# Performance work log

Measured on AMD Instinct MI355X. Metric: run time of the kernel, lower is better.

## Reference

```python
import jax, jax.numpy as jnp
import numpy as np

B, T, F, C, H = 128, 2048, 16, 8, 20  # batch, seq_len, n_features, n_channels, mlp_hidden


def _iir(u, b, rho, psi):
    """Stable 2nd-order MIMO IIR (dynoNet parametrization).
    u: [B,T,I], b: [O,I,3], rho/psi: [O,I,1] -> returns [B,T,O].
    y[t] = v[t] - a1*y[t-1] - a2*y[t-2] per (o,i) pair, summed over i.
    """
    r = jax.nn.sigmoid(rho[..., 0])            # [O,I]
    beta = jnp.pi * jax.nn.sigmoid(psi[..., 0])
    a1 = -2.0 * r * jnp.cos(beta)              # [O,I]
    a2 = r * r                                 # [O,I]
    up = jnp.pad(u, ((0, 0), (2, 0), (0, 0)))  # causal pad, up[:,2:]==u
    # FIR numerator v[b,t,o,i] = sum_k b[o,i,k] * u[b,t-k,i]
    v = (b[:, :, 0] * u[:, :, None, :]
         + b[:, :, 1] * up[:, 1:-1, None, :]
         + b[:, :, 2] * up[:, :-2, None, :])   # [B,T,O,I]

    def step(carry, vt):
        y1, y2 = carry
        y = vt - a1 * y1 - a2 * y2
        return (y, y1), y

    Bn, O, I = u.shape[0], b.shape[0], b.shape[1]
    z = jnp.zeros((Bn, O, I), u.dtype)
    _, ys = jax.lax.scan(step, (z, z), jnp.moveaxis(v, 1, 0))  # [T,B,O,I]
    return jnp.moveaxis(ys.sum(-1), 0, 1)      # [B,T,O]


def setup_inputs() -> dict:
    key = jax.random.key(0)
    ks = jax.random.split(key, 9)
    return {
        "x": jax.random.normal(ks[0], (B, T, F), jnp.float32),
        # G1: n_features -> n_channels
        "b1": 0.01 * jax.random.normal(ks[1], (C, F, 3), jnp.float32),
        "rho1": 0.1 * jax.random.normal(ks[2], (C, F, 1), jnp.float32),
        "psi1": 0.1 * jax.random.normal(ks[3], (C, F, 1), jnp.float32),
        # MLP: Linear(C,H) -> Tanh -> Linear(H,C)
        "w1": jax.random.normal(ks[4], (H, C), jnp.float32) / np.sqrt(C),
        "bias1": jnp.zeros((H,), jnp.float32),
        "w2": jax.random.normal(ks[5], (C, H), jnp.float32) / np.sqrt(H),
        "bias2": jnp.zeros((C,), jnp.float32),
        # G2: n_channels -> 1
        "b2": 0.01 * jax.random.normal(ks[6], (1, C, 3), jnp.float32),
        "rho2": 0.1 * jax.random.normal(ks[7], (1, C, 1), jnp.float32),
        "psi2": 0.1 * jax.random.normal(ks[8], (1, C, 1), jnp.float32),
    }


def reference(x, b1, rho1, psi1, w1, bias1, w2, bias2, b2, rho2, psi2):
    y1 = _iir(x, b1, rho1, psi1)                 # [B,T,C]
    h = jnp.tanh(y1 @ w1.T + bias1)              # [B,T,H]
    y2 = h @ w2.T + bias2                        # [B,T,C]
    y3 = _iir(y2, b2, rho2, psi2)                # [B,T,1]
    return y3[:, -1, :]                          # [B,1]
```

## Files before the change

kernel.cpp:

```cpp
#include <hip/hip_runtime.h>
#include <math.h>

#define BATCH 128
#define TLEN  2048
#define FDIM  16
#define CDIM  8
#define HDIM  20
#define KTAPS 64
#define XWIN  128
#define XSTR  132

__device__ float g_filt[8192 + 512];

__global__ void wh_precompute(const float* __restrict__ b1,
                              const float* __restrict__ rho1,
                              const float* __restrict__ psi1,
                              const float* __restrict__ b2,
                              const float* __restrict__ rho2,
                              const float* __restrict__ psi2) {
    int tid = threadIdx.x;
    if (tid >= 136) return;
    float c0, c1, c2, rho, psi;
    if (tid < 128) {
        int oi = tid;
        c0 = b1[oi * 3 + 0]; c1 = b1[oi * 3 + 1]; c2 = b1[oi * 3 + 2];
        rho = rho1[oi]; psi = psi1[oi];
    } else {
        int c = tid - 128;
        c0 = b2[c * 3 + 0]; c1 = b2[c * 3 + 1]; c2 = b2[c * 3 + 2];
        rho = rho2[c]; psi = psi2[c];
    }
    float r    = 1.0f / (1.0f + expf(-rho));
    float beta = 3.14159265358979323846f * (1.0f / (1.0f + expf(-psi)));
    float a1   = -2.0f * r * cosf(beta);
    float a2   = r * r;

    float ym1 = 0.0f, ym2 = 0.0f;
    for (int t = 0; t < KTAPS; ++t) {
        float v = (t == 0) ? c0 : (t == 1) ? c1 : (t == 2) ? c2 : 0.0f;
        float y = v - a1 * ym1 - a2 * ym2;
        if (tid < 128) {
            int o = tid >> 4, i = tid & 15;
            g_filt[(i * KTAPS + (KTAPS - 1 - t)) * CDIM + o] = y;
        } else {
            int c = tid - 128;
            g_filt[8192 + c * KTAPS + t] = y;
        }
        ym2 = ym1; ym1 = y;
    }
}

__global__ __launch_bounds__(256) void wh_main(const float* __restrict__ x,
                                               const float* __restrict__ w1,
                                               const float* __restrict__ bias1,
                                               const float* __restrict__ w2,
                                               const float* __restrict__ bias2,
                                               float* __restrict__ out) {
    __shared__ float xs[FDIM * XSTR];
    __shared__ float part[4 * CDIM * 64];

    const int tid  = threadIdx.x;
    const int b    = blockIdx.x;
    const int lane = tid & 63;
    const int w    = tid >> 6;

    const float* xb = x + ((size_t)b * TLEN + (TLEN - XWIN)) * FDIM;
#pragma unroll
    for (int rep = 0; rep < 2; ++rep) {
        int f4 = tid + rep * 256;
        float4 v = ((const float4*)xb)[f4];
        int lt = f4 >> 2;
        int ib = (f4 & 3) * 4;
        xs[(ib + 0) * XSTR + lt] = v.x;
        xs[(ib + 1) * XSTR + lt] = v.y;
        xs[(ib + 2) * XSTR + lt] = v.z;
        xs[(ib + 3) * XSTR + lt] = v.w;
    }
    __syncthreads();

    float acc[CDIM];
#pragma unroll
    for (int o = 0; o < CDIM; ++o) acc[o] = 0.0f;

#pragma unroll
    for (int ii = 0; ii < 4; ++ii) {
        int i = (w << 2) + ii;
        const float* xrow = &xs[i * XSTR + lane + 1];
        const float* kp = g_filt + __builtin_amdgcn_readfirstlane(i * (KTAPS * CDIM));
#pragma unroll 8
        for (int s = 0; s < KTAPS; ++s) {
            float xv = xrow[s];
#pragma unroll
            for (int o = 0; o < CDIM; ++o) acc[o] += kp[s * CDIM + o] * xv;
        }
    }

#pragma unroll
    for (int o = 0; o < CDIM; ++o) part[(w * CDIM + o) * 64 + lane] = acc[o];
    __syncthreads();

    if (w == 0) {
        float y1v[CDIM];
#pragma unroll
        for (int o = 0; o < CDIM; ++o)
            y1v[o] = part[(0 * CDIM + o) * 64 + lane] + part[(1 * CDIM + o) * 64 + lane] +
                     part[(2 * CDIM + o) * 64 + lane] + part[(3 * CDIM + o) * 64 + lane];

        float y2v[CDIM];
#pragma unroll
        for (int c = 0; c < CDIM; ++c) y2v[c] = bias2[c];
#pragma unroll
        for (int j = 0; j < HDIM; ++j) {
            float a = bias1[j];
#pragma unroll
            for (int o = 0; o < CDIM; ++o) a += w1[j * CDIM + o] * y1v[o];
            float hv = tanhf(a);
#pragma unroll
            for (int c = 0; c < CDIM; ++c) y2v[c] += w2[c * HDIM + j] * hv;
        }

        const float* h2 = g_filt + 8192;
        int tau = 63 - lane;
        float y3 = 0.0f;
#pragma unroll
        for (int c = 0; c < CDIM; ++c) y3 += h2[c * KTAPS + tau] * y2v[c];

#pragma unroll
        for (int off = 32; off > 0; off >>= 1) y3 += __shfl_down(y3, off, 64);
        if (lane == 0) out[b] = y3;
    }
}

extern "C" void kernel_launch(void* const* d_in, const int* in_sizes, int n_in,
                              void* d_out, int out_size, void* d_ws, size_t ws_size,
                              hipStream_t stream) {
    const float* x     = (const float*)d_in[0];
    const float* b1    = (const float*)d_in[1];
    const float* rho1  = (const float*)d_in[2];
    const float* psi1  = (const float*)d_in[3];
    const float* w1    = (const float*)d_in[4];
    const float* bias1 = (const float*)d_in[5];
    const float* w2    = (const float*)d_in[6];
    const float* bias2 = (const float*)d_in[7];
    const float* b2    = (const float*)d_in[8];
    const float* rho2  = (const float*)d_in[9];
    const float* psi2  = (const float*)d_in[10];
    float* out = (float*)d_out;

    wh_precompute<<<1, 256, 0, stream>>>(b1, rho1, psi1, b2, rho2, psi2);
    wh_main<<<BATCH, 256, 0, stream>>>(x, w1, bias1, w2, bias2, out);
}
```

Measured before the change: 101.8 us.

## Fuse filter impulse-response precompute into main kernel using shared memory

Removes the separate single-block precompute kernel and its global filter table. Each block now recomputes the truncated impulse responses for both IIR stages into shared memory while the input window loads are in flight. The main convolution reads the taps from LDS as float4 instead of scalar global loads. This drops one kernel launch and the dependency between the two kernels, at the cost of redundant per-block recurrence work and extra LDS usage.

New measurement: 92.75 us. -8.9%, faster.

```diff
diff --git a/kernel.cpp b/kernel.cpp
--- a/kernel.cpp
+++ b/kernel.cpp
@@ -10,52 +10,20 @@
 #define XWIN  128
 #define XSTR  132
 
-__device__ float g_filt[8192 + 512];
-
-__global__ void wh_precompute(const float* __restrict__ b1,
-                              const float* __restrict__ rho1,
-                              const float* __restrict__ psi1,
-                              const float* __restrict__ b2,
-                              const float* __restrict__ rho2,
-                              const float* __restrict__ psi2) {
-    int tid = threadIdx.x;
-    if (tid >= 136) return;
-    float c0, c1, c2, rho, psi;
-    if (tid < 128) {
-        int oi = tid;
-        c0 = b1[oi * 3 + 0]; c1 = b1[oi * 3 + 1]; c2 = b1[oi * 3 + 2];
-        rho = rho1[oi]; psi = psi1[oi];
-    } else {
-        int c = tid - 128;
-        c0 = b2[c * 3 + 0]; c1 = b2[c * 3 + 1]; c2 = b2[c * 3 + 2];
-        rho = rho2[c]; psi = psi2[c];
-    }
-    float r    = 1.0f / (1.0f + expf(-rho));
-    float beta = 3.14159265358979323846f * (1.0f / (1.0f + expf(-psi)));
-    float a1   = -2.0f * r * cosf(beta);
-    float a2   = r * r;
-
-    float ym1 = 0.0f, ym2 = 0.0f;
-    for (int t = 0; t < KTAPS; ++t) {
-        float v = (t == 0) ? c0 : (t == 1) ? c1 : (t == 2) ? c2 : 0.0f;
-        float y = v - a1 * ym1 - a2 * ym2;
-        if (tid < 128) {
-            int o = tid >> 4, i = tid & 15;
-            g_filt[(i * KTAPS + (KTAPS - 1 - t)) * CDIM + o] = y;
-        } else {
-            int c = tid - 128;
-            g_filt[8192 + c * KTAPS + t] = y;
-        }
-        ym2 = ym1; ym1 = y;
-    }
-}
-
-__global__ __launch_bounds__(256) void wh_main(const float* __restrict__ x,
-                                               const float* __restrict__ w1,
-                                               const float* __restrict__ bias1,
-                                               const float* __restrict__ w2,
-                                               const float* __restrict__ bias2,
-                                               float* __restrict__ out) {
+__global__ __launch_bounds__(256) void wh_fused(const float* __restrict__ x,
+                                                const float* __restrict__ b1,
+                                                const float* __restrict__ rho1,
+                                                const float* __restrict__ psi1,
+                                                const float* __restrict__ w1,
+                                                const float* __restrict__ bias1,
+                                                const float* __restrict__ w2,
+                                                const float* __restrict__ bias2,
+                                                const float* __restrict__ b2,
+                                                const float* __restrict__ rho2,
+                                                const float* __restrict__ psi2,
+                                                float* __restrict__ out) {
+    __shared__ float ks[KTAPS * FDIM * CDIM];
+    __shared__ float h2s[CDIM * KTAPS];
     __shared__ float xs[FDIM * XSTR];
     __shared__ float part[4 * CDIM * 64];
 
@@ -65,16 +33,56 @@
     const int w    = tid >> 6;
 
     const float* xb = x + ((size_t)b * TLEN + (TLEN - XWIN)) * FDIM;
-#pragma unroll
-    for (int rep = 0; rep < 2; ++rep) {
-        int f4 = tid + rep * 256;
-        float4 v = ((const float4*)xb)[f4];
-        int lt = f4 >> 2;
-        int ib = (f4 & 3) * 4;
-        xs[(ib + 0) * XSTR + lt] = v.x;
-        xs[(ib + 1) * XSTR + lt] = v.y;
-        xs[(ib + 2) * XSTR + lt] = v.z;
-        xs[(ib + 3) * XSTR + lt] = v.w;
+    float4 v0 = ((const float4*)xb)[tid];
+    float4 v1 = ((const float4*)xb)[tid + 256];
+
+    if (tid < 136) {
+        float c0, c1, c2, rho, psi;
+        if (tid < 128) {
+            c0 = b1[tid * 3 + 0]; c1 = b1[tid * 3 + 1]; c2 = b1[tid * 3 + 2];
+            rho = rho1[tid]; psi = psi1[tid];
+        } else {
+            int c = tid - 128;
+            c0 = b2[c * 3 + 0]; c1 = b2[c * 3 + 1]; c2 = b2[c * 3 + 2];
+            rho = rho2[c]; psi = psi2[c];
+        }
+        float r    = 1.0f / (1.0f + expf(-rho));
+        float beta = 3.14159265358979323846f * (1.0f / (1.0f + expf(-psi)));
+        float a1   = -2.0f * r * cosf(beta);
+        float a2   = r * r;
+        float ym1 = 0.0f, ym2 = 0.0f;
+        if (tid < 128) {
+            int o = tid >> 4, i = tid & 15;
+            float* dst = &ks[i * CDIM + o];
+            for (int t = 0; t < KTAPS; ++t) {
+                float v = (t == 0) ? c0 : (t == 1) ? c1 : (t == 2) ? c2 : 0.0f;
+                float y = v - a1 * ym1 - a2 * ym2;
+                dst[(KTAPS - 1 - t) * (FDIM * CDIM)] = y;
+                ym2 = ym1; ym1 = y;
+            }
+        } else {
+            int c = tid - 128;
+            for (int t = 0; t < KTAPS; ++t) {
+                float v = (t == 0) ? c0 : (t == 1) ? c1 : (t == 2) ? c2 : 0.0f;
+                float y = v - a1 * ym1 - a2 * ym2;
+                h2s[c * KTAPS + t] = y;
+                ym2 = ym1; ym1 = y;
+            }
+        }
+    }
+
+    {
+        int lt0 = tid >> 2, ib0 = (tid & 3) * 4;
+        xs[(ib0 + 0) * XSTR + lt0] = v0.x;
+        xs[(ib0 + 1) * XSTR + lt0] = v0.y;
+        xs[(ib0 + 2) * XSTR + lt0] = v0.z;
+        xs[(ib0 + 3) * XSTR + lt0] = v0.w;
+        int f4 = tid + 256;
+        int lt1 = f4 >> 2, ib1 = (f4 & 3) * 4;
+        xs[(ib1 + 0) * XSTR + lt1] = v1.x;
+        xs[(ib1 + 1) * XSTR + lt1] = v1.y;
+        xs[(ib1 + 2) * XSTR + lt1] = v1.z;
+        xs[(ib1 + 3) * XSTR + lt1] = v1.w;
     }
     __syncthreads();
 
@@ -86,12 +94,16 @@
     for (int ii = 0; ii < 4; ++ii) {
         int i = (w << 2) + ii;
         const float* xrow = &xs[i * XSTR + lane + 1];
-        const float* kp = g_filt + __builtin_amdgcn_readfirstlane(i * (KTAPS * CDIM));
+        const float* kbase = &ks[i * CDIM];
 #pragma unroll 8
         for (int s = 0; s < KTAPS; ++s) {
             float xv = xrow[s];
-#pragma unroll
-            for (int o = 0; o < CDIM; ++o) acc[o] += kp[s * CDIM + o] * xv;
+            const float4* tp = (const float4*)&kbase[s * (FDIM * CDIM)];
+            float4 t0 = tp[0], t1 = tp[1];
+            acc[0] += t0.x * xv; acc[1] += t0.y * xv;
+            acc[2] += t0.z * xv; acc[3] += t0.w * xv;
+            acc[4] += t1.x * xv; acc[5] += t1.y * xv;
+            acc[6] += t1.z * xv; acc[7] += t1.w * xv;
         }
     }
 
@@ -119,11 +131,10 @@
             for (int c = 0; c < CDIM; ++c) y2v[c] += w2[c * HDIM + j] * hv;
         }
 
-        const float* h2 = g_filt + 8192;
         int tau = 63 - lane;
         float y3 = 0.0f;
 #pragma unroll
-        for (int c = 0; c < CDIM; ++c) y3 += h2[c * KTAPS + tau] * y2v[c];
+        for (int c = 0; c < CDIM; ++c) y3 += h2s[c * KTAPS + tau] * y2v[c];
 
 #pragma unroll
         for (int off = 32; off > 0; off >>= 1) y3 += __shfl_down(y3, off, 64);
@@ -147,6 +158,6 @@
     const float* psi2  = (const float*)d_in[10];
     float* out = (float*)d_out;
 
-    wh_precompute<<<1, 256, 0, stream>>>(b1, rho1, psi1, b2, rho2, psi2);
-    wh_main<<<BATCH, 256, 0, stream>>>(x, w1, bias1, w2, bias2, out);
+    wh_fused<<<BATCH, 256, 0, stream>>>(x, b1, rho1, psi1, w1, bias1, w2, bias2,
+                                        b2, rho2, psi2, out);
 }
```
